# Kernel tuning notes

Hardware: AMD Instinct MI355X
Metric: run time of the kernel (lower is better)

The kernel has to match this reference:

```python
import jax, jax.numpy as jnp
import numpy as np

B, F, P, H, D = 2, 128, 256, 8, 64
DIM = H * D  # dim = num_heads * head_dim


def setup_inputs() -> dict:
    key = jax.random.key(0)
    ks = jax.random.split(key, 4)
    s = 0.02  # init scale for weights
    return {
        "x": jax.random.normal(ks[0], (B, F, P, DIM), jnp.float32),
        # frame QKV: projects dim -> (qkv, heads, dim_head)
        "W_f": (jax.random.normal(ks[1], (3, H, D, DIM), jnp.float32) * s),
        "b_f": jnp.zeros((3, H, D), jnp.float32),
        # point QKV: mixes (heads_in, dim_head_in) -> (qkv, heads_out, dim_head_out)
        "W_p": (jax.random.normal(ks[2], (3, H, D, H, D), jnp.float32) * s),
        "b_p": jnp.zeros((3, H, D), jnp.float32),
        # out projection: (heads, dim_head) -> dim
        "W_o": (jax.random.normal(ks[3], (H, D, DIM), jnp.float32) * s),
        "b_o": jnp.zeros((DIM,), jnp.float32),
    }


def reference(x, W_f, b_f, W_p, b_p, W_o, b_o):
    # ---- frame attention (attend across frames, per point) ----
    # qkv: [3, b, point, frame, heads, dim_head]
    qkv = jnp.einsum('bfpd,qhed->qbpfhe', x, W_f) + b_f[:, None, None, None, :, :]
    q, k, v = qkv[0], qkv[1], qkv[2]
    # scores: [b, point, frame_q, frame_k, heads]  (NOTE: source applies no 1/sqrt(d) scaling)
    scores = jnp.einsum('bpfhe,bpghe->bpfgh', q, k)
    w = jax.nn.softmax(scores, axis=3)  # softmax over frame_key
    fa = jnp.einsum('bpfgh,bpghe->bfphe', w, v)  # [b, frame, point, heads, dim_head]

    # ---- point attention (attend across points, per frame) ----
    # qkv2: [3, b, frame, point, heads, dim_head]
    qkv2 = jnp.einsum('bfpij,qheij->qbfphe', fa, W_p) + b_p[:, None, None, None, :, :]
    q2, k2, v2 = qkv2[0], qkv2[1], qkv2[2]
    # scores2: [b, frame, point_q, point_k, heads] (no scaling, per source)
    scores2 = jnp.einsum('bfphe,bfqhe->bfpqh', q2, k2)
    w2 = jax.nn.softmax(scores2, axis=3)  # softmax over point_key
    pa = jnp.einsum('bfpqh,bfqhe->bfphe', w2, v2)  # [b, frame, point, heads, dim_head]

    # ---- output projection ----
    return jnp.einsum('bfphe,hed->bfpd', pa, W_o) + b_o
```

## Files before the change

### kernel.cpp

```cpp
#include <hip/hip_runtime.h>
#include <hip/hip_bf16.h>
#include <stdint.h>

typedef __bf16 bf16;
typedef __attribute__((ext_vector_type(8))) __bf16 bf16x8;
typedef __attribute__((ext_vector_type(4))) __bf16 bf16x4;
typedef __attribute__((ext_vector_type(4))) float f32x4;

#define B_ 2
#define F_ 128
#define P_ 256
#define H_ 8
#define D_ 64
#define DIM_ 512
#define NROWS (B_*F_*P_)

__device__ __forceinline__ void load_lds16(const void* g, void* l) {
  __builtin_amdgcn_global_load_lds(
      (__attribute__((address_space(1))) void*)(uintptr_t)g,
      (__attribute__((address_space(3))) void*)(uint32_t)(uintptr_t)l,
      16, 0, 0);
}

__global__ void cvt_f32_bf16(const float* __restrict__ src, bf16* __restrict__ dst, int n)
{
  int i = (blockIdx.x * 256 + threadIdx.x) * 8;
  if (i < n) {
    float4 a = *(const float4*)(src + i);
    float4 b = *(const float4*)(src + i + 4);
    bf16x8 o;
    o[0] = (bf16)a.x; o[1] = (bf16)a.y; o[2] = (bf16)a.z; o[3] = (bf16)a.w;
    o[4] = (bf16)b.x; o[5] = (bf16)b.y; o[6] = (bf16)b.z; o[7] = (bf16)b.w;
    *(bf16x8*)(dst + i) = o;
  }
}

__global__ void transpose_wo(const float* __restrict__ src, bf16* __restrict__ dst)
{
  int idx = blockIdx.x * 256 + threadIdx.x;
  int d = idx & 511, he = idx >> 9;
  dst[(size_t)d * 512 + he] = (bf16)src[(size_t)he * 512 + d];
}

template <typename OutT, int NTn>
__global__ __launch_bounds__(512, 4)
void gemm_mn(const bf16* __restrict__ A, const bf16* __restrict__ Bt,
             const float* __restrict__ bias, OutT* __restrict__ C)
{
  constexpr int K = 512;
  constexpr int N = NTn * 128;
  constexpr int NTILES = 16;
  constexpr int BUF = 12288;
  __shared__ __align__(16) bf16 Ls[3 * BUF];

  const int t    = threadIdx.x;
  const int lane = t & 63;
  const int l16  = lane & 15;
  const int qd   = lane >> 4;
  const int wave = t >> 6;
  const int wm   = wave >> 1;
  const int wn   = wave & 1;

  constexpr int NWG = 256 * NTn;
  const int logical = (blockIdx.x & 7) * (NWG / 8) + (blockIdx.x >> 3);
  const int mBase = (logical / NTn) * 256;
  const int nBase = (logical % NTn) * 128;

  const int soct = (((t & 3) ^ ((t >> 3) & 3)) << 3);
  const bf16* aP0 = A  + (size_t)(mBase + (t >> 2)) * K + soct;
  const bf16* aP1 = aP0 + (size_t)128 * K;
  const bf16* bP  = Bt + (size_t)(nBase + (t >> 2)) * K + soct;

#define STAGE(tt) do { bf16* Lb_ = Ls + ((tt) % 3) * BUF; \
    load_lds16(aP0 + (tt) * 32, Lb_ + t * 8); \
    load_lds16(aP1 + (tt) * 32, Lb_ + 4096 + t * 8); \
    load_lds16(bP  + (tt) * 32, Lb_ + 8192 + t * 8); } while (0)

  const int swz    = ((qd ^ ((l16 >> 1) & 3)) << 3);
  const int aRdOff = (wm * 64 + l16) * 32 + swz;
  const int bRdOff = 8192 + (wn * 64 + l16) * 32 + swz;

  f32x4 acc[4][4] = {};

#define MF(i, j, av, bv) \
  acc[i][j] = __builtin_amdgcn_mfma_f32_16x16x32_bf16(av, bv, acc[i][j], 0, 0, 0)

  STAGE(0); STAGE(1);

#pragma unroll
  for (int tt = 0; tt < NTILES; ++tt) {
    if (tt + 2 < NTILES) STAGE(tt + 2);
    if      (tt <  NTILES - 2) asm volatile("s_waitcnt vmcnt(6)" ::: "memory");
    else if (tt == NTILES - 2) asm volatile("s_waitcnt vmcnt(3)" ::: "memory");
    else                       asm volatile("s_waitcnt vmcnt(0)" ::: "memory");
    __builtin_amdgcn_s_barrier();
    asm volatile("" ::: "memory");

    const bf16* Lb = Ls + (tt % 3) * BUF;
    bf16x8 a[4], b[4];
#pragma unroll
    for (int j = 0; j < 4; ++j) b[j] = *(const bf16x8*)(Lb + bRdOff + j * 512);
#pragma unroll
    for (int i = 0; i < 4; ++i) a[i] = *(const bf16x8*)(Lb + aRdOff + i * 512);

    __builtin_amdgcn_s_setprio(1);
#pragma unroll
    for (int i = 0; i < 4; ++i)
#pragma unroll
      for (int j = 0; j < 4; ++j) MF(i, j, b[j], a[i]);
    __builtin_amdgcn_s_setprio(0);

    asm volatile("s_waitcnt lgkmcnt(0)" ::: "memory");
    __builtin_amdgcn_s_barrier();
    asm volatile("" ::: "memory");
  }
#undef STAGE
#undef MF

#pragma unroll
  for (int j = 0; j < 4; ++j) {
    const int ncol = nBase + wn * 64 + j * 16 + qd * 4;
    const f32x4 bv = *(const f32x4*)(bias + ncol);
#pragma unroll
    for (int i = 0; i < 4; ++i) {
      const size_t off = (size_t)(mBase + wm * 64 + i * 16 + l16) * N + ncol;
      if constexpr (__is_same(OutT, float)) {
        f32x4 o;
#pragma unroll
        for (int r = 0; r < 4; ++r) o[r] = acc[i][j][r] + bv[r];
        *(f32x4*)(C + off) = o;
      } else {
        bf16x4 o;
#pragma unroll
        for (int r = 0; r < 4; ++r) o[r] = (bf16)(acc[i][j][r] + bv[r]);
        *(bf16x4*)(C + off) = o;
      }
    }
  }
}

template <int NKT, int MODE, int VS>
__global__ __launch_bounds__(256, 2)
void attn2(const bf16* __restrict__ qkv, bf16* __restrict__ outp)
{
  __shared__ __align__(16) bf16 Vt[64 * VS];
  __shared__ __align__(16) bf16 Pq[128 * 136];

  const int t    = threadIdx.x;
  const int lane = t & 63;
  const int wave = t >> 6;
  const int l16  = lane & 15;
  const int qd   = lane >> 4;

  const int bid = blockIdx.x;
  int h, q0, rowbase, rstride;
  if (MODE == 0) {
    h = bid & 7;
    int p = (bid >> 3) & (P_ - 1);
    int b = bid >> 11;
    rowbase = b * F_ * P_ + p; rstride = P_; q0 = 0;
  } else {
    int qb = bid & 1;
    h = (bid >> 1) & 7;
    int f = (bid >> 4) & (F_ - 1);
    int b = bid >> 11;
    rowbase = (b * F_ + f) * P_; rstride = 1; q0 = qb * 128;
  }

#pragma unroll
  for (int p = 0; p < NKT / 8; ++p) {
    int key = p * 128 + (t >> 1);
    int eh  = (t & 1) * 32;
    const bf16* src = qkv + (size_t)(rowbase + key * rstride) * 1536 + 1024 + h * 64 + eh;
    bf16x8 v[4];
#pragma unroll
    for (int jj = 0; jj < 4; ++jj) v[jj] = *(const bf16x8*)(src + jj * 8);
#pragma unroll
    for (int jj = 0; jj < 4; ++jj)
#pragma unroll
      for (int j = 0; j < 8; ++j)
        Vt[(eh + jj * 8 + j) * VS + key] = v[jj][j];
  }

  const int qloc = wave * 32;
  bf16x8 qf[2][2];
#pragma unroll
  for (int qt = 0; qt < 2; ++qt)
#pragma unroll
    for (int ks = 0; ks < 2; ++ks)
      qf[qt][ks] = *(const bf16x8*)(qkv +
          (size_t)(rowbase + (q0 + qloc + qt * 16 + l16) * rstride) * 1536 +
          h * 64 + ks * 32 + qd * 8);

  f32x4 sacc[NKT][2] = {};
#pragma unroll
  for (int tn = 0; tn < NKT; ++tn) {
    const bf16* krow = qkv + (size_t)(rowbase + (tn * 16 + l16) * rstride) * 1536 + 512 + h * 64;
    bf16x8 kf0 = *(const bf16x8*)(krow + qd * 8);
    bf16x8 kf1 = *(const bf16x8*)(krow + 32 + qd * 8);
#pragma unroll
    for (int qt = 0; qt < 2; ++qt) {
      sacc[tn][qt] = __builtin_amdgcn_mfma_f32_16x16x32_bf16(kf0, qf[qt][0], sacc[tn][qt], 0, 0, 0);
      sacc[tn][qt] = __builtin_amdgcn_mfma_f32_16x16x32_bf16(kf1, qf[qt][1], sacc[tn][qt], 0, 0, 0);
    }
  }

#pragma unroll
  for (int qt = 0; qt < 2; ++qt) {
    float m = -3.0e38f;
#pragma unroll
    for (int tn = 0; tn < NKT; ++tn)
#pragma unroll
      for (int r = 0; r < 4; ++r) m = fmaxf(m, sacc[tn][qt][r]);
    m = fmaxf(m, __shfl_xor(m, 16));
    m = fmaxf(m, __shfl_xor(m, 32));
    float s = 0.0f;
#pragma unroll
    for (int tn = 0; tn < NKT; ++tn)
#pragma unroll
      for (int r = 0; r < 4; ++r) {
        float e0 = __expf(sacc[tn][qt][r] - m);
        sacc[tn][qt][r] = e0;
        s += e0;
      }
    s += __shfl_xor(s, 16);
    s += __shfl_xor(s, 32);
    float inv = 1.0f / s;
#pragma unroll
    for (int tn = 0; tn < NKT; ++tn)
#pragma unroll
      for (int r = 0; r < 4; ++r) sacc[tn][qt][r] *= inv;
  }

  f32x4 oacc[4][2] = {};
#pragma unroll
  for (int hf = 0; hf < NKT / 8; ++hf) {
#pragma unroll
    for (int qt = 0; qt < 2; ++qt)
#pragma unroll
      for (int tl = 0; tl < 8; ++tl) {
        int tn = hf * 8 + tl;
        bf16x4 pk;
#pragma unroll
        for (int r = 0; r < 4; ++r) pk[r] = (bf16)sacc[tn][qt][r];
        *(bf16x4*)(Pq + (qloc + qt * 16 + l16) * 136 + tl * 16 + qd * 4) = pk;
      }
    if (hf == 0) __syncthreads();
#pragma unroll
    for (int ks = 0; ks < 4; ++ks) {
      bf16x8 pf[2];
#pragma unroll
      for (int qt = 0; qt < 2; ++qt)
        pf[qt] = *(const bf16x8*)(Pq + (qloc + qt * 16 + l16) * 136 + ks * 32 + qd * 8);
#pragma unroll
      for (int te = 0; te < 4; ++te) {
        bf16x8 vf = *(const bf16x8*)(Vt + (te * 16 + l16) * VS + hf * 128 + ks * 32 + qd * 8);
#pragma unroll
        for (int qt = 0; qt < 2; ++qt)
          oacc[te][qt] = __builtin_amdgcn_mfma_f32_16x16x32_bf16(vf, pf[qt], oacc[te][qt], 0, 0, 0);
      }
    }
  }

#pragma unroll
  for (int te = 0; te < 4; ++te)
#pragma unroll
    for (int qt = 0; qt < 2; ++qt) {
      int q = q0 + qloc + qt * 16 + l16;
      bf16x4 pk;
#pragma unroll
      for (int r = 0; r < 4; ++r) pk[r] = (bf16)oacc[te][qt][r];
      *(bf16x4*)(outp + (size_t)(rowbase + q * rstride) * 512 + h * 64 + te * 16 + qd * 4) = pk;
    }
}

extern "C" void kernel_launch(void* const* d_in, const int* in_sizes, int n_in,
                              void* d_out, int out_size, void* d_ws, size_t ws_size,
                              hipStream_t stream)
{
  (void)in_sizes; (void)n_in; (void)out_size; (void)ws_size;
  const float* x   = (const float*)d_in[0];
  const float* Wf  = (const float*)d_in[1];
  const float* bfb = (const float*)d_in[2];
  const float* Wp  = (const float*)d_in[3];
  const float* bpb = (const float*)d_in[4];
  const float* Wo  = (const float*)d_in[5];
  const float* bob = (const float*)d_in[6];
  float* out = (float*)d_out;

  char* ws = (char*)d_ws;
  bf16* qkv = (bf16*)ws;
  bf16* fa  = (bf16*)(ws + (size_t)NROWS * 1536 * 2);
  bf16* xb  = fa;
  char* wbase = ws + (size_t)NROWS * 1536 * 2 + (size_t)NROWS * 512 * 2;
  bf16* wfb = (bf16*)wbase;
  bf16* wpb = (bf16*)(wbase + 1536 * 512 * 2);
  bf16* wot = (bf16*)(wbase + 2 * 1536 * 512 * 2);

  cvt_f32_bf16<<<(NROWS * 512) / (256 * 8), 256, 0, stream>>>(x, xb, NROWS * 512);
  cvt_f32_bf16<<<(1536 * 512) / (256 * 8), 256, 0, stream>>>(Wf, wfb, 1536 * 512);
  cvt_f32_bf16<<<(1536 * 512) / (256 * 8), 256, 0, stream>>>(Wp, wpb, 1536 * 512);
  transpose_wo<<<1024, 256, 0, stream>>>(Wo, wot);

  gemm_mn<bf16, 12><<<3072, 512, 0, stream>>>(xb, wfb, bfb, qkv);
  attn2<8, 0, 136><<<4096, 256, 0, stream>>>(qkv, fa);
  gemm_mn<bf16, 12><<<3072, 512, 0, stream>>>(fa, wpb, bpb, qkv);
  attn2<16, 1, 272><<<4096, 256, 0, stream>>>(qkv, fa);
  gemm_mn<float, 4><<<1024, 512, 0, stream>>>(fa, wot, bob, out);
}
```

Baseline: 783.5 us.

## Load GEMM B operand directly into registers instead of staging through LDS

The weight (B) tile is no longer copied into shared memory. Each wave loads its B fragments straight from global memory into double-buffered registers, one k-tile ahead, and the LDS buffer shrinks to hold only A. This removes LDS traffic and ds_read work for B and cuts the LDS footprint, which may raise occupancy. The cost is that the waves sharing a B tile now each read it from global or L2 separately, and register pressure goes up. The vmcnt accounting was changed to match the new load counts.

```diff
diff --git a/kernel.cpp b/kernel.cpp
--- a/kernel.cpp
+++ b/kernel.cpp
@@ -50,7 +50,7 @@
   constexpr int K = 512;
   constexpr int N = NTn * 128;
   constexpr int NTILES = 16;
-  constexpr int BUF = 12288;
+  constexpr int BUF = 8192;
   __shared__ __align__(16) bf16 Ls[3 * BUF];
 
   const int t    = threadIdx.x;
@@ -67,39 +67,54 @@
   const int nBase = (logical % NTn) * 128;
 
   const int soct = (((t & 3) ^ ((t >> 3) & 3)) << 3);
-  const bf16* aP0 = A  + (size_t)(mBase + (t >> 2)) * K + soct;
+  const bf16* aP0 = A + (size_t)(mBase + (t >> 2)) * K + soct;
   const bf16* aP1 = aP0 + (size_t)128 * K;
-  const bf16* bP  = Bt + (size_t)(nBase + (t >> 2)) * K + soct;
-
-#define STAGE(tt) do { bf16* Lb_ = Ls + ((tt) % 3) * BUF; \
+
+#define STAGE_A(tt) do { bf16* Lb_ = Ls + ((tt) % 3) * BUF; \
     load_lds16(aP0 + (tt) * 32, Lb_ + t * 8); \
-    load_lds16(aP1 + (tt) * 32, Lb_ + 4096 + t * 8); \
-    load_lds16(bP  + (tt) * 32, Lb_ + 8192 + t * 8); } while (0)
+    load_lds16(aP1 + (tt) * 32, Lb_ + 4096 + t * 8); } while (0)
+
+  const bf16* bBase = Bt + (size_t)nBase * K;
+  int boff[4];
+#pragma unroll
+  for (int j = 0; j < 4; ++j)
+    boff[j] = (wn * 64 + j * 16 + l16) * K + qd * 8;
 
   const int swz    = ((qd ^ ((l16 >> 1) & 3)) << 3);
   const int aRdOff = (wm * 64 + l16) * 32 + swz;
-  const int bRdOff = 8192 + (wn * 64 + l16) * 32 + swz;
 
   f32x4 acc[4][4] = {};
+  bf16x8 bfr[2][4];
 
 #define MF(i, j, av, bv) \
   acc[i][j] = __builtin_amdgcn_mfma_f32_16x16x32_bf16(av, bv, acc[i][j], 0, 0, 0)
 
-  STAGE(0); STAGE(1);
+#pragma unroll
+  for (int j = 0; j < 4; ++j) bfr[0][j] = *(const bf16x8*)(bBase + boff[j]);
+  __builtin_amdgcn_sched_barrier(0);
+  STAGE_A(0); STAGE_A(1);
+  asm volatile("s_waitcnt vmcnt(2)" ::: "memory");
+  __builtin_amdgcn_s_barrier();
+  asm volatile("" ::: "memory");
 
 #pragma unroll
   for (int tt = 0; tt < NTILES; ++tt) {
-    if (tt + 2 < NTILES) STAGE(tt + 2);
-    if      (tt <  NTILES - 2) asm volatile("s_waitcnt vmcnt(6)" ::: "memory");
-    else if (tt == NTILES - 2) asm volatile("s_waitcnt vmcnt(3)" ::: "memory");
+    const int cur = tt & 1, nxt = cur ^ 1;
+
+    if (tt + 2 < NTILES) STAGE_A(tt + 2);
+    if (tt + 1 < NTILES) {
+#pragma unroll
+      for (int j = 0; j < 4; ++j)
+        bfr[nxt][j] = *(const bf16x8*)(bBase + boff[j] + (tt + 1) * 32);
+    }
+    if      (tt <= NTILES - 3) asm volatile("s_waitcnt vmcnt(6)" ::: "memory");
+    else if (tt == NTILES - 2) asm volatile("s_waitcnt vmcnt(4)" ::: "memory");
     else                       asm volatile("s_waitcnt vmcnt(0)" ::: "memory");
     __builtin_amdgcn_s_barrier();
     asm volatile("" ::: "memory");
 
     const bf16* Lb = Ls + (tt % 3) * BUF;
-    bf16x8 a[4], b[4];
-#pragma unroll
-    for (int j = 0; j < 4; ++j) b[j] = *(const bf16x8*)(Lb + bRdOff + j * 512);
+    bf16x8 a[4];
 #pragma unroll
     for (int i = 0; i < 4; ++i) a[i] = *(const bf16x8*)(Lb + aRdOff + i * 512);
 
@@ -107,14 +122,14 @@
 #pragma unroll
     for (int i = 0; i < 4; ++i)
 #pragma unroll
-      for (int j = 0; j < 4; ++j) MF(i, j, b[j], a[i]);
+      for (int j = 0; j < 4; ++j) MF(i, j, bfr[cur][j], a[i]);
     __builtin_amdgcn_s_setprio(0);
 
     asm volatile("s_waitcnt lgkmcnt(0)" ::: "memory");
     __builtin_amdgcn_s_barrier();
     asm volatile("" ::: "memory");
   }
-#undef STAGE
+#undef STAGE_A
 #undef MF
 
 #pragma unroll
```

After: 1.034 ms. 1.32x slower.
